# Optimization experiments

Hardware: AMD Instinct MI355X
Metric: run time of the kernel (lower is better)

## Reference

```python
import jax, jax.numpy as jnp
import numpy as np
import math


def _selective_scan(u, delta, A, Bs, Cs, D, delta_bias):
    """Mamba selective scan.
    u, delta: (B,K,Dn,L); A: (K,Dn,N); Bs, Cs: (B,K,N,L); D, delta_bias: (K,Dn).
    delta_softplus=True semantics from selective_scan_fn.
    """
    delta = jax.nn.softplus(delta + delta_bias[None, :, :, None])
    dl = jnp.moveaxis(delta, -1, 0)  # (L,B,K,Dn)
    ul = jnp.moveaxis(u, -1, 0)      # (L,B,K,Dn)
    bl = jnp.moveaxis(Bs, -1, 0)     # (L,B,K,N)
    cl = jnp.moveaxis(Cs, -1, 0)     # (L,B,K,N)
    h0 = jnp.zeros(u.shape[:3] + (A.shape[-1],), u.dtype)  # (B,K,Dn,N)

    def step(h, inp):
        d, ut, bt, ct = inp
        h = jnp.exp(d[..., None] * A) * h + (d * ut)[..., None] * bt[:, :, None, :]
        y = jnp.einsum('bkdn,bkn->bkd', h, ct)
        return h, y

    _, ys = jax.lax.scan(step, h0, (dl, ul, bl, cl))
    return jnp.moveaxis(ys, 0, -1) + D[None, :, :, None] * u  # (B,K,Dn,L)


def setup_inputs() -> dict:
    key = jax.random.key(0)
    B, H, W, C = 8, 64, 64, 192
    Dn, N, R, K = 192, 8, 12, 4
    ks = jax.random.split(key, 8)
    x = jax.random.normal(ks[0], (B, H, W, C), jnp.float32)
    in_proj_w = jax.random.normal(ks[1], (2 * Dn, C), jnp.float32) * (C ** -0.5)
    conv_w = jax.random.normal(ks[2], (Dn, 1, 3, 3), jnp.float32) * 0.2
    conv_b = jnp.zeros((Dn,), jnp.float32)
    x_proj_w = jax.random.normal(ks[3], (K, R + 2 * N, Dn), jnp.float32) * (Dn ** -0.5)
    dt_std = R ** -0.5
    dt_projs_w = jax.random.uniform(ks[4], (K, Dn, R), jnp.float32, -dt_std, dt_std)
    dt = jnp.exp(jax.random.uniform(ks[5], (K, Dn), jnp.float32)
                 * (math.log(0.1) - math.log(0.001)) + math.log(0.001))
    dt = jnp.clip(dt, 1e-4, None)
    dt_projs_b = dt + jnp.log(-jnp.expm1(-dt))  # inverse softplus
    A_logs = jnp.broadcast_to(jnp.log(jnp.arange(1, N + 1, dtype=jnp.float32)), (K, Dn, N)).copy()
    Ds = jnp.ones((K, Dn), jnp.float32)
    ln_w = jnp.ones((Dn,), jnp.float32)
    ln_b = jnp.zeros((Dn,), jnp.float32)
    out_proj_w = jax.random.normal(ks[6], (C, Dn), jnp.float32) * (Dn ** -0.5)
    return {"x": x, "in_proj_w": in_proj_w, "conv_w": conv_w, "conv_b": conv_b,
            "x_proj_w": x_proj_w, "dt_projs_w": dt_projs_w, "dt_projs_b": dt_projs_b,
            "A_logs": A_logs, "Ds": Ds, "ln_w": ln_w, "ln_b": ln_b,
            "out_proj_w": out_proj_w}


def reference(x, in_proj_w, conv_w, conv_b, x_proj_w, dt_projs_w, dt_projs_b,
              A_logs, Ds, ln_w, ln_b, out_proj_w):
    B, H, W, C = x.shape
    K, _, Dn = x_proj_w.shape
    N = A_logs.shape[-1]
    R = dt_projs_w.shape[-1]
    L = H * W

    xz = x @ in_proj_w.T                       # (B,H,W,2*Dn)
    xf, z = jnp.split(xz, 2, axis=-1)
    xc = jnp.transpose(xf, (0, 3, 1, 2))       # (B,Dn,H,W)
    xc = jax.lax.conv_general_dilated(
        xc, conv_w, (1, 1), [(1, 1), (1, 1)],
        feature_group_count=Dn,
        dimension_numbers=('NCHW', 'OIHW', 'NCHW')) + conv_b[None, :, None, None]
    xc = jax.nn.silu(xc)

    # 4-directional scan sequences: hw, wh, reversed-hw, reversed-wh
    x_hw = xc.reshape(B, Dn, L)
    x_wh = jnp.transpose(xc, (0, 1, 3, 2)).reshape(B, Dn, L)
    x2 = jnp.stack([x_hw, x_wh], axis=1)
    xs = jnp.concatenate([x2, jnp.flip(x2, axis=-1)], axis=1)  # (B,4,Dn,L)

    x_dbl = jnp.einsum('bkdl,kcd->bkcl', xs, x_proj_w)
    dts, Bsx, Csx = jnp.split(x_dbl, [R, R + N], axis=2)
    dts = jnp.einsum('bkrl,kdr->bkdl', dts, dt_projs_w)

    A = -jnp.exp(A_logs)                       # (K,Dn,N)
    out_y = _selective_scan(xs, dts, A, Bsx, Csx, Ds, dt_projs_b)  # (B,4,Dn,L)

    inv_y = jnp.flip(out_y[:, 2:4], axis=-1)
    wh_y = jnp.transpose(out_y[:, 1].reshape(B, Dn, W, H), (0, 1, 3, 2)).reshape(B, Dn, L)
    invwh_y = jnp.transpose(inv_y[:, 1].reshape(B, Dn, W, H), (0, 1, 3, 2)).reshape(B, Dn, L)
    y = out_y[:, 0] + inv_y[:, 0] + wh_y + invwh_y  # (B,Dn,L)

    y = jnp.transpose(y, (0, 2, 1)).reshape(B, H, W, Dn)
    mu = y.mean(-1, keepdims=True)
    var = y.var(-1, keepdims=True)
    y = (y - mu) / jnp.sqrt(var + 1e-5) * ln_w + ln_b
    y = y * jax.nn.silu(z)
    return y @ out_proj_w.T
```

## Files before the change

### kernel.cpp

```cpp
#include <hip/hip_runtime.h>
#include <hip/hip_bf16.h>

constexpr int B_  = 8;
constexpr int H_  = 64;
constexpr int W_  = 64;
constexpr int C_  = 192;
constexpr int Dn  = 192;
constexpr int Nst = 8;
constexpr int R_  = 12;
constexpr int K_  = 4;
constexpr int L_  = H_ * W_;
constexpr int CS  = 64;
constexpr int NC  = L_ / CS;
constexpr int CPROJ = R_ + 2 * Nst;
constexpr int MROWS = B_ * L_;

typedef __attribute__((ext_vector_type(8))) short short8v;
typedef __attribute__((ext_vector_type(4))) float f32x4;

__device__ __forceinline__ int map_t(int k, int t) {
    int tt = (k >= 2) ? (L_ - 1 - t) : t;
    if (k & 1) tt = (tt & 63) * 64 + (tt >> 6);
    return tt;
}

__device__ __forceinline__ short f2bf(float f) {
    unsigned u = __float_as_uint(f);
    u += 0x7FFFu + ((u >> 16) & 1u);
    return (short)(u >> 16);
}
__device__ __forceinline__ float bf2f(short s) {
    return __uint_as_float(((unsigned)(unsigned short)s) << 16);
}

constexpr int WOFF_IN  = 0;
constexpr int WOFF_XP  = 73728;
constexpr int WOFF_OUT = 95232;
constexpr int WTOTAL   = 132096;
constexpr int XUNITS   = MROWS * Dn / 8;
constexpr int WUNITS   = WTOTAL / 8;
__global__ __launch_bounds__(256) void k_cvt(const float* __restrict__ x,
                                             const float* __restrict__ w_in,
                                             const float* __restrict__ xpw,
                                             const float* __restrict__ wout,
                                             short* __restrict__ x_bf,
                                             short* __restrict__ w_bf) {
    int g = blockIdx.x * 256 + threadIdx.x;
    const float* src;
    short* dst;
    int off;
    if (g < XUNITS) { src = x; dst = x_bf; off = g * 8; }
    else {
        g -= XUNITS;
        if (g >= WUNITS) return;
        int base = g * 8;
        dst = w_bf; off = base;
        if (base < WOFF_XP)       { src = w_in; }
        else if (base < WOFF_OUT) { src = xpw;  src -= WOFF_XP; }
        else                      { src = wout; src -= WOFF_OUT; }
    }
    float4 a = *reinterpret_cast<const float4*>(src + off);
    float4 b = *reinterpret_cast<const float4*>(src + off + 4);
    short8v v = {f2bf(a.x), f2bf(a.y), f2bf(a.z), f2bf(a.w),
                 f2bf(b.x), f2bf(b.y), f2bf(b.z), f2bf(b.w)};
    *reinterpret_cast<short8v*>(dst + off) = v;
}

__device__ __forceinline__ void mgemm_core(const short* __restrict__ A,
                                           const short* __restrict__ Wb,
                                           f32x4 (&acc)[4][2],
                                           int mrow, int ncol, int Nact, int K) {
    const int lane = threadIdx.x & 63;
    const int koff = (lane >> 4) * 8;
    for (int k0 = 0; k0 < K; k0 += 32) {
        short8v af[4], bfr[2];
#pragma unroll
        for (int mf = 0; mf < 4; mf++)
            af[mf] = *reinterpret_cast<const short8v*>(
                A + (size_t)(mrow + mf * 16) * K + k0 + koff);
#pragma unroll
        for (int nf = 0; nf < 2; nf++) {
            int r = ncol + nf * 16;
            short8v z = {0, 0, 0, 0, 0, 0, 0, 0};
            bfr[nf] = (r < Nact)
                ? *reinterpret_cast<const short8v*>(Wb + (size_t)r * K + k0 + koff)
                : z;
        }
#pragma unroll
        for (int mf = 0; mf < 4; mf++)
#pragma unroll
            for (int nf = 0; nf < 2; nf++)
                acc[mf][nf] = __builtin_amdgcn_mfma_f32_16x16x32_bf16(
                    af[mf], bfr[nf], acc[mf][nf], 0, 0, 0);
    }
}

__global__ __launch_bounds__(256) void k_mgemm_f(const short* __restrict__ A,
                                                 const short* __restrict__ Wb,
                                                 float* __restrict__ out0,
                                                 int Nact, int K) {
    const int m0 = blockIdx.x * 128, n0 = blockIdx.y * 64;
    const int wid = threadIdx.x >> 6, lane = threadIdx.x & 63;
    const int wm = wid >> 1, wn = wid & 1;
    f32x4 acc[4][2] = {};
    mgemm_core(A, Wb, acc, m0 + wm * 64 + (lane & 15), n0 + wn * 32 + (lane & 15),
               Nact, K);
    const int prow = (lane >> 4) * 4, pcol = lane & 15;
#pragma unroll
    for (int mf = 0; mf < 4; mf++) {
        int mbase = m0 + wm * 64 + mf * 16 + prow;
#pragma unroll
        for (int nf = 0; nf < 2; nf++) {
            int n = n0 + wn * 32 + nf * 16 + pcol;
            if (n >= Nact) continue;
#pragma unroll
            for (int r = 0; r < 4; r++)
                out0[(size_t)(mbase + r) * Nact + n] = acc[mf][nf][r];
        }
    }
}

__global__ __launch_bounds__(256) void k_mgemm_in(const short* __restrict__ A,
                                                  const short* __restrict__ Wb,
                                                  short* __restrict__ xf_bf,
                                                  short* __restrict__ z_bf,
                                                  int K) {
    const int m0 = blockIdx.x * 128, n0 = blockIdx.y * 64;
    const int wid = threadIdx.x >> 6, lane = threadIdx.x & 63;
    const int wm = wid >> 1, wn = wid & 1;
    f32x4 acc[4][2] = {};
    mgemm_core(A, Wb, acc, m0 + wm * 64 + (lane & 15), n0 + wn * 32 + (lane & 15),
               384, K);
    const int prow = (lane >> 4) * 4, pcol = lane & 15;
#pragma unroll
    for (int mf = 0; mf < 4; mf++) {
        int mbase = m0 + wm * 64 + mf * 16 + prow;
#pragma unroll
        for (int nf = 0; nf < 2; nf++) {
            int n = n0 + wn * 32 + nf * 16 + pcol;
#pragma unroll
            for (int r = 0; r < 4; r++) {
                int m = mbase + r;
                if (n < 192) xf_bf[(size_t)m * 192 + n] = f2bf(acc[mf][nf][r]);
                else         z_bf[(size_t)m * 192 + (n - 192)] = f2bf(acc[mf][nf][r]);
            }
        }
    }
}

__global__ __launch_bounds__(256) void k_conv(const short* __restrict__ xfb,
                                              const float* __restrict__ cw,
                                              const float* __restrict__ cb,
                                              short* __restrict__ xcb) {
    size_t i = (size_t)blockIdx.x * 256 + threadIdx.x;
    int d = (int)(i % Dn);
    int p = (int)(i / Dn);
    int w = p & 63; p >>= 6;
    int h = p & 63; p >>= 6;
    int b = p;
    float acc = cb[d];
#pragma unroll
    for (int kh = 0; kh < 3; kh++) {
        int hh = h + kh - 1;
        if (hh < 0 || hh >= H_) continue;
#pragma unroll
        for (int kw = 0; kw < 3; kw++) {
            int ww = w + kw - 1;
            if (ww < 0 || ww >= W_) continue;
            acc = fmaf(bf2f(xfb[(((size_t)b * H_ + hh) * W_ + ww) * Dn + d]),
                       cw[d * 9 + kh * 3 + kw], acc);
        }
    }
    float sig = 1.f / (1.f + __expf(-acc));
    xcb[i] = f2bf(acc * sig);
}

__device__ __forceinline__ void delta_e1(float x, float& delta, float& e1) {
    if (x > 20.f) { delta = x; e1 = __expf(-x); }
    else {
        float t = __expf(x);
        delta = __logf(1.f + t);
        e1 = __builtin_amdgcn_rcpf(1.f + t);
    }
}

__device__ __forceinline__ float dot12(const float4& a, const float4& b,
                                       const float4& c, const float* w, float x) {
    x = fmaf(a.x, w[0], x);  x = fmaf(a.y, w[1], x);
    x = fmaf(a.z, w[2], x);  x = fmaf(a.w, w[3], x);
    x = fmaf(b.x, w[4], x);  x = fmaf(b.y, w[5], x);
    x = fmaf(b.z, w[6], x);  x = fmaf(b.w, w[7], x);
    x = fmaf(c.x, w[8], x);  x = fmaf(c.y, w[9], x);
    x = fmaf(c.z, w[10], x); x = fmaf(c.w, w[11], x);
    return x;
}

__global__ __launch_bounds__(192) void k_scan1(const short* __restrict__ xcb,
                                               const float* __restrict__ xdbl,
                                               const float* __restrict__ dtw_all,
                                               const float* __restrict__ dtb_all,
                                               const float* __restrict__ alog,
                                               float* __restrict__ Aprod,
                                               float* __restrict__ hpart) {
    const int blk = blockIdx.x;
    const int c = blk % NC;
    const int k = (blk / NC) % K_;
    const int b = blk / (NC * K_);
    const int d = threadIdx.x;
    const int t0 = c * CS;

    __shared__ float4 sx4[CS][5];
    const float4* xd4 = reinterpret_cast<const float4*>(xdbl);
    for (int i = d; i < CS * 5; i += 192) {
        int ts = i / 5, q = i % 5;
        sx4[ts][q] = xd4[((size_t)b * L_ + map_t(k, t0 + ts)) * 28 + k * 7 + q];
    }
    __syncthreads();

    float dtw[R_];
#pragma unroll
    for (int r = 0; r < R_; r++) dtw[r] = dtw_all[((size_t)k * Dn + d) * R_ + r];
    const float bias = dtb_all[k * Dn + d];
    float Av[Nst];
    bool fast = true;
#pragma unroll
    for (int n = 0; n < Nst; n++) {
        Av[n] = -__expf(alog[((size_t)k * Dn + d) * Nst + n]);
        fast = fast && (fabsf(Av[n] + (float)(n + 1)) < 1e-3f);
    }

    float h[Nst] = {};
    float Ap[Nst];
#pragma unroll
    for (int n = 0; n < Nst; n++) Ap[n] = 1.f;
    float e1p = 1.f;

    float u_next = bf2f(xcb[((size_t)b * L_ + map_t(k, t0)) * Dn + d]);
    if (fast) {
        for (int ts = 0; ts < CS; ts++) {
            float u = u_next;
            if (ts + 1 < CS) u_next = bf2f(xcb[((size_t)b * L_ + map_t(k, t0 + ts + 1)) * Dn + d]);
            float4 q0 = sx4[ts][0], q1 = sx4[ts][1], q2 = sx4[ts][2];
            float4 qb0 = sx4[ts][3], qb1 = sx4[ts][4];
            float delta, e1; delta_e1(dot12(q0, q1, q2, dtw, bias), delta, e1);
            float du = delta * u;
            e1p *= e1;
            float a2 = e1 * e1, a3 = a2 * e1, a4 = a2 * a2;
            float a5 = a4 * e1, a6 = a4 * a2, a7 = a4 * a3, a8 = a4 * a4;
            h[0] = fmaf(e1, h[0], du * qb0.x);
            h[1] = fmaf(a2, h[1], du * qb0.y);
            h[2] = fmaf(a3, h[2], du * qb0.z);
            h[3] = fmaf(a4, h[3], du * qb0.w);
            h[4] = fmaf(a5, h[4], du * qb1.x);
            h[5] = fmaf(a6, h[5], du * qb1.y);
            h[6] = fmaf(a7, h[6], du * qb1.z);
            h[7] = fmaf(a8, h[7], du * qb1.w);
        }
        float p2 = e1p * e1p, p3 = p2 * e1p, p4 = p2 * p2;
        Ap[0] = e1p; Ap[1] = p2; Ap[2] = p3; Ap[3] = p4;
        Ap[4] = p4 * e1p; Ap[5] = p4 * p2; Ap[6] = p4 * p3; Ap[7] = p4 * p4;
    } else {
        for (int ts = 0; ts < CS; ts++) {
            float u = u_next;
            if (ts + 1 < CS) u_next = bf2f(xcb[((size_t)b * L_ + map_t(k, t0 + ts + 1)) * Dn + d]);
            float4 q0 = sx4[ts][0], q1 = sx4[ts][1], q2 = sx4[ts][2];
            float4 qb0 = sx4[ts][3], qb1 = sx4[ts][4];
            float Bv[Nst] = {qb0.x, qb0.y, qb0.z, qb0.w, qb1.x, qb1.y, qb1.z, qb1.w};
            float delta, e1; delta_e1(dot12(q0, q1, q2, dtw, bias), delta, e1);
            float du = delta * u;
#pragma unroll
            for (int n = 0; n < Nst; n++) {
                float a = __expf(delta * Av[n]);
                Ap[n] *= a;
                h[n] = fmaf(a, h[n], du * Bv[n]);
            }
        }
    }
    size_t base = ((((size_t)(b * K_ + k) * NC + c) * Dn + d)) * Nst;
#pragma unroll
    for (int n = 0; n < Nst; n++) { Aprod[base + n] = Ap[n]; hpart[base + n] = h[n]; }
}

__global__ __launch_bounds__(256) void k_scan2(const float* __restrict__ Aprod,
                                               const float* __restrict__ hpart,
                                               float* __restrict__ hin) {
    int idx = blockIdx.x * 256 + threadIdx.x;
    int dn = idx % (Dn * Nst);
    int bk = idx / (Dn * Nst);
    size_t stride = (size_t)Dn * Nst;
    size_t base = (size_t)bk * NC * stride + dn;
    float h = 0.f;
    for (int cc = 0; cc < NC; cc++) {
        size_t s = base + (size_t)cc * stride;
        hin[s] = h;
        h = fmaf(Aprod[s], h, hpart[s]);
    }
}

__global__ __launch_bounds__(192) void k_scan3(const short* __restrict__ xcb,
                                               const float* __restrict__ xdbl,
                                               const float* __restrict__ dtw_all,
                                               const float* __restrict__ dtb_all,
                                               const float* __restrict__ alog,
                                               const float* __restrict__ dvec,
                                               const float* __restrict__ hin,
                                               short* __restrict__ y0,
                                               short* __restrict__ y1,
                                               short* __restrict__ y2,
                                               short* __restrict__ y3) {
    const int blk = blockIdx.x;
    const int c = blk % NC;
    const int k = (blk / NC) % K_;
    const int b = blk / (NC * K_);
    const int d = threadIdx.x;
    const int t0 = c * CS;
    short* __restrict__ yk = (k == 0) ? y0 : (k == 1) ? y1 : (k == 2) ? y2 : y3;

    __shared__ float4 sx4[CS][7];
    const float4* xd4 = reinterpret_cast<const float4*>(xdbl);
    for (int i = d; i < CS * 7; i += 192) {
        int ts = i / 7, q = i % 7;
        sx4[ts][q] = xd4[((size_t)b * L_ + map_t(k, t0 + ts)) * 28 + k * 7 + q];
    }
    __syncthreads();

    float dtw[R_];
#pragma unroll
    for (int r = 0; r < R_; r++) dtw[r] = dtw_all[((size_t)k * Dn + d) * R_ + r];
    const float bias = dtb_all[k * Dn + d];
    const float Dk = dvec[k * Dn + d];
    float Av[Nst];
    bool fast = true;
#pragma unroll
    for (int n = 0; n < Nst; n++) {
        Av[n] = -__expf(alog[((size_t)k * Dn + d) * Nst + n]);
        fast = fast && (fabsf(Av[n] + (float)(n + 1)) < 1e-3f);
    }

    size_t hbase = ((((size_t)(b * K_ + k) * NC + c) * Dn + d)) * Nst;
    float h[Nst];
#pragma unroll
    for (int n = 0; n < Nst; n++) h[n] = hin[hbase + n];

    int lm = map_t(k, t0);
    float u_next = bf2f(xcb[((size_t)b * L_ + lm) * Dn + d]);
    if (fast) {
        for (int ts = 0; ts < CS; ts++) {
            int lm_cur = lm;
            float u = u_next;
            if (ts + 1 < CS) {
                lm = map_t(k, t0 + ts + 1);
                u_next = bf2f(xcb[((size_t)b * L_ + lm) * Dn + d]);
            }
            float4 q0 = sx4[ts][0], q1 = sx4[ts][1], q2 = sx4[ts][2];
            float4 qb0 = sx4[ts][3], qb1 = sx4[ts][4];
            float4 qc0 = sx4[ts][5], qc1 = sx4[ts][6];
            float delta, e1; delta_e1(dot12(q0, q1, q2, dtw, bias), delta, e1);
            float du = delta * u;
            float a2 = e1 * e1, a3 = a2 * e1, a4 = a2 * a2;
            float a5 = a4 * e1, a6 = a4 * a2, a7 = a4 * a3, a8 = a4 * a4;
            h[0] = fmaf(e1, h[0], du * qb0.x);
            h[1] = fmaf(a2, h[1], du * qb0.y);
            h[2] = fmaf(a3, h[2], du * qb0.z);
            h[3] = fmaf(a4, h[3], du * qb0.w);
            h[4] = fmaf(a5, h[4], du * qb1.x);
            h[5] = fmaf(a6, h[5], du * qb1.y);
            h[6] = fmaf(a7, h[6], du * qb1.z);
            h[7] = fmaf(a8, h[7], du * qb1.w);
            float y = h[0] * qc0.x;
            y = fmaf(h[1], qc0.y, y);
            y = fmaf(h[2], qc0.z, y);
            y = fmaf(h[3], qc0.w, y);
            y = fmaf(h[4], qc1.x, y);
            y = fmaf(h[5], qc1.y, y);
            y = fmaf(h[6], qc1.z, y);
            y = fmaf(h[7], qc1.w, y);
            yk[((size_t)b * L_ + lm_cur) * Dn + d] = f2bf(fmaf(Dk, u, y));
        }
    } else {
        for (int ts = 0; ts < CS; ts++) {
            int lm_cur = lm;
            float u = u_next;
            if (ts + 1 < CS) {
                lm = map_t(k, t0 + ts + 1);
                u_next = bf2f(xcb[((size_t)b * L_ + lm) * Dn + d]);
            }
            float4 q0 = sx4[ts][0], q1 = sx4[ts][1], q2 = sx4[ts][2];
            float4 qb0 = sx4[ts][3], qb1 = sx4[ts][4];
            float4 qc0 = sx4[ts][5], qc1 = sx4[ts][6];
            float Bv[Nst] = {qb0.x, qb0.y, qb0.z, qb0.w, qb1.x, qb1.y, qb1.z, qb1.w};
            float Cv[Nst] = {qc0.x, qc0.y, qc0.z, qc0.w, qc1.x, qc1.y, qc1.z, qc1.w};
            float delta, e1; delta_e1(dot12(q0, q1, q2, dtw, bias), delta, e1);
            float du = delta * u;
            float y = 0.f;
#pragma unroll
            for (int n = 0; n < Nst; n++) {
                float a = __expf(delta * Av[n]);
                h[n] = fmaf(a, h[n], du * Bv[n]);
                y = fmaf(h[n], Cv[n], y);
            }
            yk[((size_t)b * L_ + lm_cur) * Dn + d] = f2bf(fmaf(Dk, u, y));
        }
    }
}

__global__ __launch_bounds__(256) void k_ln(const short* __restrict__ y0,
                                            const short* __restrict__ y1,
                                            const short* __restrict__ y2,
                                            const short* __restrict__ y3,
                                            const short* __restrict__ zb,
                                            const float* __restrict__ lnw,
                                            const float* __restrict__ lnb,
                                            short* __restrict__ yfin) {
    const int row = blockIdx.x * 4 + (threadIdx.x >> 6);
    const int lane = threadIdx.x & 63;
    const size_t base = (size_t)row * Dn;
    float v[3];
    float s = 0.f, s2 = 0.f;
#pragma unroll
    for (int j = 0; j < 3; j++) {
        size_t idx = base + lane + j * 64;
        v[j] = bf2f(y0[idx]) + bf2f(y1[idx]) + bf2f(y2[idx]) + bf2f(y3[idx]);
        s += v[j];
        s2 = fmaf(v[j], v[j], s2);
    }
#pragma unroll
    for (int o = 1; o < 64; o <<= 1) {
        s += __shfl_xor(s, o);
        s2 += __shfl_xor(s2, o);
    }
    const float inv = 1.f / 192.f;
    float mu = s * inv;
    float var = s2 * inv - mu * mu;
    float rstd = rsqrtf(var + 1e-5f);
#pragma unroll
    for (int j = 0; j < 3; j++) {
        int dd = lane + j * 64;
        size_t idx = base + dd;
        float zz = bf2f(zb[idx]);
        float sig = 1.f / (1.f + __expf(-zz));
        float res = ((v[j] - mu) * rstd * lnw[dd] + lnb[dd]) * (zz * sig);
        yfin[idx] = f2bf(res);
    }
}

extern "C" void kernel_launch(void* const* d_in, const int* in_sizes, int n_in,
                              void* d_out, int out_size, void* d_ws, size_t ws_size,
                              hipStream_t stream) {
    const float* x    = (const float*)d_in[0];
    const float* w_in = (const float*)d_in[1];
    const float* cw   = (const float*)d_in[2];
    const float* cb   = (const float*)d_in[3];
    const float* xpw  = (const float*)d_in[4];
    const float* dtw  = (const float*)d_in[5];
    const float* dtb  = (const float*)d_in[6];
    const float* alog = (const float*)d_in[7];
    const float* dvec = (const float*)d_in[8];
    const float* lnw  = (const float*)d_in[9];
    const float* lnb  = (const float*)d_in[10];
    const float* wout = (const float*)d_in[11];
    float* out = (float*)d_out;

    const size_t SH  = (size_t)MROWS * Dn;
    const size_t SCN = (size_t)B_ * K_ * NC * Dn * Nst;

    char* p = (char*)d_ws;
    short* x_bf  = (short*)p; p += SH * 2;
    short* xf_bf = (short*)p; p += SH * 2;
    short* z_bf  = (short*)p; p += SH * 2;
    short* xc_bf = (short*)p; p += SH * 2;
    float* xdbl  = (float*)p; p += (size_t)MROWS * (K_ * CPROJ) * 4;
    float* Aprod = (float*)p; p += SCN * 4;
    float* hpart = (float*)p; p += SCN * 4;
    float* hin   = (float*)p; p += SCN * 4;
    short* w_bf  = (short*)p;
    short* y0 = x_bf;
    short* y1 = xf_bf;
    short* y2 = (short*)Aprod;
    short* y3 = (short*)hpart;
    short* yfin_bf = (short*)hin;

    k_cvt<<<(XUNITS + WUNITS + 255) / 256, 256, 0, stream>>>(x, w_in, xpw, wout,
                                                             x_bf, w_bf);
    k_mgemm_in<<<dim3(MROWS / 128, 6), 256, 0, stream>>>(x_bf, w_bf + WOFF_IN,
                                                         xf_bf, z_bf, C_);
    k_conv<<<(int)(SH / 256), 256, 0, stream>>>(xf_bf, cw, cb, xc_bf);
    k_mgemm_f<<<dim3(MROWS / 128, 2), 256, 0, stream>>>(xc_bf, w_bf + WOFF_XP,
                                                        xdbl, K_ * CPROJ, Dn);
    k_scan1<<<B_ * K_ * NC, 192, 0, stream>>>(xc_bf, xdbl, dtw, dtb, alog, Aprod, hpart);
    k_scan2<<<(B_ * K_ * Dn * Nst) / 256, 256, 0, stream>>>(Aprod, hpart, hin);
    k_scan3<<<B_ * K_ * NC, 192, 0, stream>>>(xc_bf, xdbl, dtw, dtb, alog, dvec,
                                              hin, y0, y1, y2, y3);
    k_ln<<<MROWS / 4, 256, 0, stream>>>(y0, y1, y2, y3, z_bf, lnw, lnb, yfin_bf);
    k_mgemm_f<<<dim3(MROWS / 128, 3), 256, 0, stream>>>(yfin_bf, w_bf + WOFF_OUT,
                                                        out, C_, Dn);
}
```

Measured before the change: 251.9 us.

## Halve scan chunk size and replace per-step index mapping with pointer strides

Reduces the chunk length of the chunked selective scan from 64 to 32, doubling the number of blocks so each serial per-thread recurrence is shorter and more blocks can run concurrently. The per-timestep map_t address computation is replaced by a constant stride pointer walk for u loads and y stores. The trade-off is twice as many chunk carries to combine in the inter-chunk pass and more partial-state traffic.

```diff
diff --git a/kernel.cpp b/kernel.cpp
--- a/kernel.cpp
+++ b/kernel.cpp
@@ -10,7 +10,7 @@
 constexpr int R_  = 12;
 constexpr int K_  = 4;
 constexpr int L_  = H_ * W_;
-constexpr int CS  = 64;
+constexpr int CS  = 32;
 constexpr int NC  = L_ / CS;
 constexpr int CPROJ = R_ + 2 * Nst;
 constexpr int MROWS = B_ * L_;
@@ -208,12 +208,14 @@
     const int b = blk / (NC * K_);
     const int d = threadIdx.x;
     const int t0 = c * CS;
+    const int stride = ((k & 1) ? 64 : 1) * ((k >= 2) ? -1 : 1);
+    const int lm0 = map_t(k, t0);
 
     __shared__ float4 sx4[CS][5];
     const float4* xd4 = reinterpret_cast<const float4*>(xdbl);
     for (int i = d; i < CS * 5; i += 192) {
         int ts = i / 5, q = i % 5;
-        sx4[ts][q] = xd4[((size_t)b * L_ + map_t(k, t0 + ts)) * 28 + k * 7 + q];
+        sx4[ts][q] = xd4[((size_t)b * L_ + lm0 + ts * stride) * 28 + k * 7 + q];
     }
     __syncthreads();
 
@@ -235,11 +237,14 @@
     for (int n = 0; n < Nst; n++) Ap[n] = 1.f;
     float e1p = 1.f;
 
-    float u_next = bf2f(xcb[((size_t)b * L_ + map_t(k, t0)) * Dn + d]);
+    const long stepD = (long)stride * Dn;
+    const short* up = xcb + ((size_t)b * L_ + lm0) * Dn + d;
+    float u_next = bf2f(*up);
     if (fast) {
         for (int ts = 0; ts < CS; ts++) {
             float u = u_next;
-            if (ts + 1 < CS) u_next = bf2f(xcb[((size_t)b * L_ + map_t(k, t0 + ts + 1)) * Dn + d]);
+            up += stepD;
+            if (ts + 1 < CS) u_next = bf2f(*up);
             float4 q0 = sx4[ts][0], q1 = sx4[ts][1], q2 = sx4[ts][2];
             float4 qb0 = sx4[ts][3], qb1 = sx4[ts][4];
             float delta, e1; delta_e1(dot12(q0, q1, q2, dtw, bias), delta, e1);
@@ -262,7 +267,8 @@
     } else {
         for (int ts = 0; ts < CS; ts++) {
             float u = u_next;
-            if (ts + 1 < CS) u_next = bf2f(xcb[((size_t)b * L_ + map_t(k, t0 + ts + 1)) * Dn + d]);
+            up += stepD;
+            if (ts + 1 < CS) u_next = bf2f(*up);
             float4 q0 = sx4[ts][0], q1 = sx4[ts][1], q2 = sx4[ts][2];
             float4 qb0 = sx4[ts][3], qb1 = sx4[ts][4];
             float Bv[Nst] = {qb0.x, qb0.y, qb0.z, qb0.w, qb1.x, qb1.y, qb1.z, qb1.w};
@@ -314,13 +320,15 @@
     const int b = blk / (NC * K_);
     const int d = threadIdx.x;
     const int t0 = c * CS;
+    const int stride = ((k & 1) ? 64 : 1) * ((k >= 2) ? -1 : 1);
+    const int lm0 = map_t(k, t0);
     short* __restrict__ yk = (k == 0) ? y0 : (k == 1) ? y1 : (k == 2) ? y2 : y3;
 
     __shared__ float4 sx4[CS][7];
     const float4* xd4 = reinterpret_cast<const float4*>(xdbl);
     for (int i = d; i < CS * 7; i += 192) {
         int ts = i / 7, q = i % 7;
-        sx4[ts][q] = xd4[((size_t)b * L_ + map_t(k, t0 + ts)) * 28 + k * 7 + q];
+        sx4[ts][q] = xd4[((size_t)b * L_ + lm0 + ts * stride) * 28 + k * 7 + q];
     }
     __syncthreads();
 
@@ -342,16 +350,15 @@
 #pragma unroll
     for (int n = 0; n < Nst; n++) h[n] = hin[hbase + n];
 
-    int lm = map_t(k, t0);
-    float u_next = bf2f(xcb[((size_t)b * L_ + lm) * Dn + d]);
+    const long stepD = (long)stride * Dn;
+    const short* up = xcb + ((size_t)b * L_ + lm0) * Dn + d;
+    short* yp = yk + ((size_t)b * L_ + lm0) * Dn + d;
+    float u_next = bf2f(*up);
     if (fast) {
         for (int ts = 0; ts < CS; ts++) {
-            int lm_cur = lm;
             float u = u_next;
-            if (ts + 1 < CS) {
-                lm = map_t(k, t0 + ts + 1);
-                u_next = bf2f(xcb[((size_t)b * L_ + lm) * Dn + d]);
-            }
+            up += stepD;
+            if (ts + 1 < CS) u_next = bf2f(*up);
             float4 q0 = sx4[ts][0], q1 = sx4[ts][1], q2 = sx4[ts][2];
             float4 qb0 = sx4[ts][3], qb1 = sx4[ts][4];
             float4 qc0 = sx4[ts][5], qc1 = sx4[ts][6];
@@ -375,16 +382,14 @@
             y = fmaf(h[5], qc1.y, y);
             y = fmaf(h[6], qc1.z, y);
             y = fmaf(h[7], qc1.w, y);
-            yk[((size_t)b * L_ + lm_cur) * Dn + d] = f2bf(fmaf(Dk, u, y));
+            *yp = f2bf(fmaf(Dk, u, y));
+            yp += stepD;
         }
     } else {
         for (int ts = 0; ts < CS; ts++) {
-            int lm_cur = lm;
             float u = u_next;
-            if (ts + 1 < CS) {
-                lm = map_t(k, t0 + ts + 1);
-                u_next = bf2f(xcb[((size_t)b * L_ + lm) * Dn + d]);
-            }
+            up += stepD;
+            if (ts + 1 < CS) u_next = bf2f(*up);
             float4 q0 = sx4[ts][0], q1 = sx4[ts][1], q2 = sx4[ts][2];
             float4 qb0 = sx4[ts][3], qb1 = sx4[ts][4];
             float4 qc0 = sx4[ts][5], qc1 = sx4[ts][6];
@@ -399,7 +404,8 @@
                 h[n] = fmaf(a, h[n], du * Bv[n]);
                 y = fmaf(h[n], Cv[n], y);
             }
-            yk[((size_t)b * L_ + lm_cur) * Dn + d] = f2bf(fmaf(Dk, u, y));
+            *yp = f2bf(fmaf(Dk, u, y));
+            yp += stepD;
         }
     }
 }
```

Result: faster. 237.7 us (-5.7%).
